# Performance work log

Hardware: AMD Instinct MI355X
Metric: run time of the kernel (lower is better)

Reference implementation:

```python
import jax, jax.numpy as jnp
import numpy as np

B, DIM = 64, 1024

def setup_inputs() -> dict:
    key = jax.random.key(0)
    ks = jax.random.split(key, 16)
    d = {
        'x': jax.random.normal(ks[0], (B, DIM), jnp.float32),
        'C': jax.random.normal(ks[1], (B, DIM, DIM), jnp.float32) * 0.02,
        'n': jax.random.normal(ks[2], (B, DIM), jnp.float32),
        'm': jax.random.normal(ks[3], (B, DIM), jnp.float32),
    }
    s = 1.0 / np.sqrt(DIM)
    names = ['q', 'k', 'v', 'i', 'f', 'o']
    for j, nm in enumerate(names):
        d['W' + nm] = jax.random.uniform(ks[4 + 2 * j], (DIM, DIM), jnp.float32, -s, s)
        d['b' + nm] = jax.random.uniform(ks[5 + 2 * j], (DIM,), jnp.float32, -s, s)
    return d

def _lin(x, W, b):
    # torch nn.Linear: x @ W.T + b
    return x @ W.T + b

def reference(x, C, n, m, Wq, bq, Wk, bk, Wv, bv, Wi, bi, Wf, bf, Wo, bo):
    q = _lin(x, Wq, bq)                      # [B, D]
    k = _lin(x, Wk, bk) / jnp.sqrt(jnp.float32(DIM))
    v = _lin(x, Wv, bv)
    i_t = _lin(x, Wi, bi)
    f_t = _lin(x, Wf, bf)
    m_new = jnp.maximum(f_t + m, i_t)        # [B, D]
    i = jnp.exp(i_t - m_new)                 # [B, D]
    f = jnp.exp(f_t + m - m_new)             # [B, D]
    # rank-1 covariance update: C_new[b,r,c] = f[b,r]*C[b,r,c] + i[b,r]*v[b,r]*k[b,c]
    C_new = f[:, :, None] * C + (i * v)[:, :, None] * k[:, None, :]
    n_new = f * n + i * k
    h = jax.nn.sigmoid(_lin(x, Wo, bo)) * jnp.einsum('brc,bc->br', C_new, q)
    return (h, C_new, n_new, m_new)
```

## Files before the change

kernel.cpp:

```cpp
#include <hip/hip_runtime.h>
#include <hip/hip_bf16.h>
#include <math.h>

#define BATCH 64
#define DIM 1024
#define NROW (BATCH * DIM)
#define OFF_H 0
#define OFF_C 65536
#define OFF_N (65536 + 67108864)
#define OFF_M (OFF_N + 65536)

typedef float f4     __attribute__((ext_vector_type(4)));
typedef float f32x4  __attribute__((ext_vector_type(4)));
typedef short bf16x8 __attribute__((ext_vector_type(8)));


__device__ inline short f2bf(float v) {
    __hip_bfloat16 h = __float2bfloat16(v);
    short s;
    __builtin_memcpy(&s, &h, 2);
    return s;
}

__device__ inline bf16x8 load_bf8(const float* __restrict__ p) {
    f4 a = *reinterpret_cast<const f4*>(p);
    f4 b = *reinterpret_cast<const f4*>(p + 4);
    bf16x8 r;
    r[0] = f2bf(a.x); r[1] = f2bf(a.y); r[2] = f2bf(a.z); r[3] = f2bf(a.w);
    r[4] = f2bf(b.x); r[5] = f2bf(b.y); r[6] = f2bf(b.z); r[7] = f2bf(b.w);
    return r;
}

__global__ __launch_bounds__(256) void gemm6_mfma(
    const float* __restrict__ x,
    const float* __restrict__ Wq, const float* __restrict__ bq,
    const float* __restrict__ Wk, const float* __restrict__ bk,
    const float* __restrict__ Wv, const float* __restrict__ bv,
    const float* __restrict__ Wi, const float* __restrict__ bi,
    const float* __restrict__ Wf, const float* __restrict__ bf_,
    const float* __restrict__ Wo, const float* __restrict__ bo,
    float* __restrict__ pre)
{
    const int bx = blockIdx.x;
    const int g  = bx >> 6;
    const int j0 = (bx & 63) << 4;
    const float* W; const float* bias;
    switch (g) {
        case 0: W = Wq; bias = bq; break;
        case 1: W = Wk; bias = bk; break;
        case 2: W = Wv; bias = bv; break;
        case 3: W = Wi; bias = bi; break;
        case 4: W = Wf; bias = bf_; break;
        default: W = Wo; bias = bo; break;
    }

    const int wave = threadIdx.x >> 6;
    const int lane = threadIdx.x & 63;
    const int l15  = lane & 15;
    const int kq   = lane >> 4;

    const float* xrow = x + (size_t)(wave * 16 + l15) * DIM + kq * 8;
    const float* wrow = W + (size_t)(j0 + l15) * DIM + kq * 8;

    f32x4 acc0 = {0.f, 0.f, 0.f, 0.f};
    f32x4 acc1 = {0.f, 0.f, 0.f, 0.f};
    #pragma unroll 4
    for (int kt = 0; kt < 32; kt += 2) {
        bf16x8 a0 = load_bf8(xrow + kt * 32);
        bf16x8 b0 = load_bf8(wrow + kt * 32);
        bf16x8 a1 = load_bf8(xrow + kt * 32 + 32);
        bf16x8 b1 = load_bf8(wrow + kt * 32 + 32);
        acc0 = __builtin_amdgcn_mfma_f32_16x16x32_bf16(a0, b0, acc0, 0, 0, 0);
        acc1 = __builtin_amdgcn_mfma_f32_16x16x32_bf16(a1, b1, acc1, 0, 0, 0);
    }
    acc0 += acc1;

    const float bv_ = bias[j0 + l15];
    float* dst = pre + (size_t)g * NROW + (size_t)(wave * 16 + kq * 4) * DIM + j0 + l15;
    #pragma unroll
    for (int r = 0; r < 4; ++r)
        dst[(size_t)r * DIM] = acc0[r] + bv_;
}

__global__ __launch_bounds__(256) void cupdate(
    const float* __restrict__ C,
    const float* __restrict__ n_in, const float* __restrict__ m_in,
    const float* __restrict__ ws,
    float* __restrict__ out)
{
    const int row  = blockIdx.x * 4 + (threadIdx.x >> 6);
    const int lane = threadIdx.x & 63;
    const int b    = row >> 10;

    const float ip  = ws[3 * NROW + row];
    const float fp_ = ws[4 * NROW + row];
    const float op  = ws[5 * NROW + row];
    const float vp  = ws[2 * NROW + row];
    const float mo  = m_in[row];

    const float mn  = fmaxf(fp_ + mo, ip);
    const float iex = expf(ip - mn);
    const float fex = expf(fp_ + mo - mn);
    const float so  = 1.f / (1.f + expf(-op));
    const float iv  = iex * vp;

    const f4* k4 = reinterpret_cast<const f4*>(ws + 1 * NROW + b * DIM);
    const f4* q4 = reinterpret_cast<const f4*>(ws + 0 * NROW + b * DIM);
    const f4* C4 = reinterpret_cast<const f4*>(C) + (size_t)row * 256;
    f4*       O4 = reinterpret_cast<f4*>(out + OFF_C) + (size_t)row * 256;

    const float ksc = iv * 0.03125f;

    float dot = 0.f;
    #pragma unroll
    for (int i = 0; i < 4; ++i) {
        const int c4 = lane + 64 * i;
        f4 cv = __builtin_nontemporal_load(&C4[c4]);
        f4 kv = k4[c4];
        f4 qv = q4[c4];
        f4 cn = fex * cv + ksc * kv;
        __builtin_nontemporal_store(cn, &O4[c4]);
        f4 pr = cn * qv;
        dot += pr.x + pr.y + pr.z + pr.w;
    }
    #pragma unroll
    for (int off = 32; off > 0; off >>= 1)
        dot += __shfl_xor(dot, off, 64);

    if (lane == 0) {
        out[OFF_H + row] = so * dot;
        const float no   = n_in[row];
        const float kp_r = ws[1 * NROW + row] * 0.03125f;
        out[OFF_N + row] = fex * no + iex * kp_r;
        out[OFF_M + row] = mn;
    }
}

extern "C" void kernel_launch(void* const* d_in, const int* in_sizes, int n_in,
                              void* d_out, int out_size, void* d_ws, size_t ws_size,
                              hipStream_t stream) {
    const float* x = (const float*)d_in[0];
    const float* C = (const float*)d_in[1];
    const float* n = (const float*)d_in[2];
    const float* m = (const float*)d_in[3];
    float* ws  = (float*)d_ws;
    float* out = (float*)d_out;

    gemm6_mfma<<<384, 256, 0, stream>>>(
        x,
        (const float*)d_in[4],  (const float*)d_in[5],
        (const float*)d_in[6],  (const float*)d_in[7],
        (const float*)d_in[8],  (const float*)d_in[9],
        (const float*)d_in[10], (const float*)d_in[11],
        (const float*)d_in[12], (const float*)d_in[13],
        (const float*)d_in[14], (const float*)d_in[15],
        ws);
    cupdate<<<NROW / 4, 256, 0, stream>>>(C, n, m, ws, out);
}
```

Baseline: 129.6 us.

## Process eight rows per wave with register-resident k/q and C prefetch

The C-update kernel now gives each wave eight consecutive rows instead of one. The k and q vectors are loaded once into registers and reused across those rows. The next row's C is prefetched while the current row is processed, and the h dot product is rewritten as fex*(C·q) + ksc*(k·q), which takes the dot off the store path. The nontemporal load and store hints are dropped and the grid shrinks to 2048 blocks, which may reduce memory-level parallelism for this bandwidth-bound stream.

```diff
diff --git a/kernel.cpp b/kernel.cpp
--- a/kernel.cpp
+++ b/kernel.cpp
@@ -82,57 +82,76 @@
         dst[(size_t)r * DIM] = acc0[r] + bv_;
 }
 
-__global__ __launch_bounds__(256) void cupdate(
+__global__ __launch_bounds__(256) void cupdate2(
     const float* __restrict__ C,
     const float* __restrict__ n_in, const float* __restrict__ m_in,
     const float* __restrict__ ws,
     float* __restrict__ out)
 {
-    const int row  = blockIdx.x * 4 + (threadIdx.x >> 6);
-    const int lane = threadIdx.x & 63;
-    const int b    = row >> 10;
+    const int blk  = blockIdx.x;
+    const int b    = blk >> 5;
+    const int rg   = blk & 31;
+    const int tid  = threadIdx.x;
+    const int w    = tid >> 6;
+    const int lane = tid & 63;
 
-    const float ip  = ws[3 * NROW + row];
-    const float fp_ = ws[4 * NROW + row];
-    const float op  = ws[5 * NROW + row];
-    const float vp  = ws[2 * NROW + row];
-    const float mo  = m_in[row];
+    const f4* k4g = reinterpret_cast<const f4*>(ws + 1 * NROW + b * DIM);
+    const f4* q4g = reinterpret_cast<const f4*>(ws + 0 * NROW + b * DIM);
+    f4 k0 = k4g[lane],       k1 = k4g[lane + 64],
+       k2 = k4g[lane + 128], k3 = k4g[lane + 192];
+    f4 q0 = q4g[lane],       q1 = q4g[lane + 64],
+       q2 = q4g[lane + 128], q3 = q4g[lane + 192];
 
-    const float mn  = fmaxf(fp_ + mo, ip);
-    const float iex = expf(ip - mn);
-    const float fex = expf(fp_ + mo - mn);
-    const float so  = 1.f / (1.f + expf(-op));
-    const float iv  = iex * vp;
-
-    const f4* k4 = reinterpret_cast<const f4*>(ws + 1 * NROW + b * DIM);
-    const f4* q4 = reinterpret_cast<const f4*>(ws + 0 * NROW + b * DIM);
-    const f4* C4 = reinterpret_cast<const f4*>(C) + (size_t)row * 256;
-    f4*       O4 = reinterpret_cast<f4*>(out + OFF_C) + (size_t)row * 256;
-
-    const float ksc = iv * 0.03125f;
-
-    float dot = 0.f;
-    #pragma unroll
-    for (int i = 0; i < 4; ++i) {
-        const int c4 = lane + 64 * i;
-        f4 cv = __builtin_nontemporal_load(&C4[c4]);
-        f4 kv = k4[c4];
-        f4 qv = q4[c4];
-        f4 cn = fex * cv + ksc * kv;
-        __builtin_nontemporal_store(cn, &O4[c4]);
-        f4 pr = cn * qv;
-        dot += pr.x + pr.y + pr.z + pr.w;
-    }
+    f4 pp = k0 * q0 + k1 * q1 + k2 * q2 + k3 * q3;
+    float kqdot = pp.x + pp.y + pp.z + pp.w;
     #pragma unroll
     for (int off = 32; off > 0; off >>= 1)
-        dot += __shfl_xor(dot, off, 64);
+        kqdot += __shfl_xor(kqdot, off, 64);
 
-    if (lane == 0) {
-        out[OFF_H + row] = so * dot;
-        const float no   = n_in[row];
-        const float kp_r = ws[1 * NROW + row] * 0.03125f;
-        out[OFF_N + row] = fex * no + iex * kp_r;
-        out[OFF_M + row] = mn;
+    const int row0 = b * DIM + rg * 32 + w * 8;
+    const f4* Cb = reinterpret_cast<const f4*>(C) + (size_t)row0 * 256;
+    f4*       Ob = reinterpret_cast<f4*>(out + OFF_C) + (size_t)row0 * 256;
+
+    f4 c0 = Cb[lane], c1 = Cb[lane + 64], c2 = Cb[lane + 128], c3 = Cb[lane + 192];
+
+    #pragma unroll
+    for (int r = 0; r < 8; ++r) {
+        const int row = row0 + r;
+        f4 p0, p1, p2, p3;
+        if (r < 7) {
+            const f4* Cn = Cb + (size_t)(r + 1) * 256;
+            p0 = Cn[lane]; p1 = Cn[lane + 64]; p2 = Cn[lane + 128]; p3 = Cn[lane + 192];
+        }
+        const float ip  = ws[3 * NROW + row];
+        const float fp_ = ws[4 * NROW + row];
+        const float op  = ws[5 * NROW + row];
+        const float vp  = ws[2 * NROW + row];
+        const float mo  = m_in[row];
+
+        const float mn  = fmaxf(fp_ + mo, ip);
+        const float iex = expf(ip - mn);
+        const float fex = expf(fp_ + mo - mn);
+        const float so  = 1.f / (1.f + expf(-op));
+        const float ksc = iex * vp * 0.03125f;
+
+        f4* Or = Ob + (size_t)r * 256;
+        Or[lane]       = fex * c0 + ksc * k0;
+        Or[lane + 64]  = fex * c1 + ksc * k1;
+        Or[lane + 128] = fex * c2 + ksc * k2;
+        Or[lane + 192] = fex * c3 + ksc * k3;
+
+        f4 d = c0 * q0 + c1 * q1 + c2 * q2 + c3 * q3;
+        float dot = d.x + d.y + d.z + d.w;
+        #pragma unroll
+        for (int off = 32; off > 0; off >>= 1)
+            dot += __shfl_xor(dot, off, 64);
+
+        if (lane == 0) {
+            out[OFF_H + row] = so * (fex * dot + ksc * kqdot);
+            out[OFF_N + row] = fex * n_in[row] + iex * ws[1 * NROW + row] * 0.03125f;
+            out[OFF_M + row] = mn;
+        }
+        c0 = p0; c1 = p1; c2 = p2; c3 = p3;
     }
 }
 
@@ -155,5 +174,5 @@
         (const float*)d_in[12], (const float*)d_in[13],
         (const float*)d_in[14], (const float*)d_in[15],
         ws);
-    cupdate<<<NROW / 4, 256, 0, stream>>>(C, n, m, ws, out);
+    cupdate2<<<2048, 256, 0, stream>>>(C, n, m, ws, out);
 }
```

Measured after the change: 136.7 us. +5.5%, slower.
